# Optimization experiments

Hardware: AMD Instinct MI355X
Metric: run time of the kernel (lower is better)

## Reference

```python
import jax, jax.numpy as jnp
import numpy as np

B, S, D, H = 4, 2048, 512, 8
HD = D // H
POOL_HEADS = 8


def setup_inputs() -> dict:
    key = jax.random.key(0)
    ks = iter(jax.random.split(key, 32))
    p = {}
    p['x'] = jax.random.normal(next(ks), (B, S, D), dtype=jnp.float32)
    p['mask'] = jnp.zeros((B, S), dtype=jnp.float32)  # key_padding_mask (1.0 = padded)
    s = 1.0 / np.sqrt(D)
    for layer in ('1', '2'):
        for name in ('q', 'k', 'v', 'o'):
            p[f'{name}{layer}_w'] = jax.random.normal(next(ks), (D, D), dtype=jnp.float32) * s
            p[f'{name}{layer}_b'] = jnp.zeros((D,), dtype=jnp.float32)
    p['ln1_g'] = jnp.ones((D,), jnp.float32); p['ln1_b'] = jnp.zeros((D,), jnp.float32)
    p['ffn_w1'] = jax.random.normal(next(ks), (D, D), dtype=jnp.float32) * s
    p['ffn_b1'] = jnp.zeros((D,), jnp.float32)
    p['ffn_w2'] = jax.random.normal(next(ks), (D, D), dtype=jnp.float32) * s
    p['ffn_b2'] = jnp.zeros((D,), jnp.float32)
    p['ln2_g'] = jnp.ones((D,), jnp.float32); p['ln2_b'] = jnp.zeros((D,), jnp.float32)
    p['pool_w'] = jax.random.normal(next(ks), (D, POOL_HEADS), dtype=jnp.float32) * s
    p['pool_b'] = jnp.zeros((POOL_HEADS,), jnp.float32)
    return p


def _layernorm(x, g, b, eps=1e-5):
    mu = jnp.mean(x, axis=-1, keepdims=True)
    var = jnp.var(x, axis=-1, keepdims=True)
    return (x - mu) * jax.lax.rsqrt(var + eps) * g + b


def _mha(x, mask, qw, qb, kw, kb, vw, vb, ow, ob):
    b, s, d = x.shape
    q = (x @ qw + qb).reshape(b, s, H, HD)
    k = (x @ kw + kb).reshape(b, s, H, HD)
    v = (x @ vw + vb).reshape(b, s, H, HD)
    scores = jnp.einsum('bihd,bjhd->bhij', q, k) / jnp.sqrt(jnp.float32(HD))
    scores = scores - mask[:, None, None, :] * 1e30  # key_padding_mask
    w = jax.nn.softmax(scores, axis=-1)  # dropout is identity at eval
    out = jnp.einsum('bhij,bjhd->bihd', w, v).reshape(b, s, d)
    return out @ ow + ob


def _pool(x, mask, pw, pb):
    alpha = jax.nn.leaky_relu(x @ pw + pb)            # [B,S,POOL_HEADS]
    alpha = alpha + mask[:, :, None] * -1e16
    alpha = jax.nn.softmax(alpha, axis=1)             # softmax over sequence
    # sum over heads of alpha_h * x, then sum over sequence
    return jnp.einsum('bs,bsd->bd', alpha.sum(axis=-1), x)


def reference(x, mask,
              q1_w, q1_b, k1_w, k1_b, v1_w, v1_b, o1_w, o1_b,
              q2_w, q2_b, k2_w, k2_b, v2_w, v2_b, o2_w, o2_b,
              ln1_g, ln1_b, ffn_w1, ffn_b1, ffn_w2, ffn_b2,
              ln2_g, ln2_b, pool_w, pool_b):
    # F.normalize(x, p=2, dim=-1)
    x = x / jnp.maximum(jnp.linalg.norm(x, axis=-1, keepdims=True), 1e-12)
    h = _mha(x, mask, q1_w, q1_b, k1_w, k1_b, v1_w, v1_b, o1_w, o1_b)
    h = _layernorm(h, ln1_g, ln1_b)
    h = jax.nn.relu(h @ ffn_w1 + ffn_b1) @ ffn_w2 + ffn_b2
    h = _mha(h, mask, q2_w, q2_b, k2_w, k2_b, v2_w, v2_b, o2_w, o2_b)
    h = _layernorm(h, ln2_g, ln2_b)
    return _pool(h, mask, pool_w, pool_b)  # [B, D] patch_feature (cls=False -> logit is None)
```

## Files before the change

### kernel.cpp

```cpp
#include <hip/hip_runtime.h>
#include <hip/hip_bf16.h>
#include <stdint.h>

#define DEVI __device__ __forceinline__

typedef float f32x4 __attribute__((ext_vector_type(4)));
typedef float f32x16 __attribute__((ext_vector_type(16)));
typedef short bf16x8 __attribute__((ext_vector_type(8)));

typedef __attribute__((address_space(3))) unsigned int as3_u32;
typedef __attribute__((address_space(1))) unsigned int as1_u32;

DEVI void gload16(const void* g, void* l) {
  __builtin_amdgcn_global_load_lds((const as1_u32*)g, (as3_u32*)l, 16, 0, 0);
}

DEVI unsigned short bf16r(float f) {
  union { float f; unsigned int u; } v; v.f = f;
  unsigned int u = v.u;
  return (unsigned short)((u + 0x7FFFu + ((u >> 16) & 1u)) >> 16);
}

DEVI float bf2f(unsigned short u) {
  unsigned int x = ((unsigned int)u) << 16;
  union { unsigned int u; float f; } v; v.u = x;
  return v.f;
}

DEVI unsigned int pkbf16(float a, float b) {
  __hip_bfloat162 h = __float22bfloat162_rn(make_float2(a, b));
  return *(unsigned int*)&h;
}

struct PrepArgs {
  const float* w[10];
  const float* b1[3];
  const float* b2[3];
};

__global__ __launch_bounds__(256) void prep_kernel(PrepArgs pa, unsigned short* wt,
                                                   float* qb1, float* qb2) {
  __shared__ float lt[64][65];
  const int slot = blockIdx.z;
  const int n0 = blockIdx.x * 64, k0 = blockIdx.y * 64;
  const float* W = pa.w[slot];
  for (int it = 0; it < 16; it++) {
    int idx = it * 256 + threadIdx.x;
    int kr = idx >> 6, nc = idx & 63;
    lt[kr][nc] = W[(long)(k0 + kr) * 512 + n0 + nc];
  }
  __syncthreads();
  unsigned short* dst = wt + (long)slot * 512 * 512;
  for (int it = 0; it < 16; it++) {
    int idx = it * 256 + threadIdx.x;
    int nr = idx >> 6, kc = idx & 63;
    dst[(long)(n0 + nr) * 512 + k0 + kc] = bf16r(lt[kc][nr]);
  }
  if (blockIdx.x == 0 && blockIdx.y == 0) {
    if (slot < 3) {
      for (int i = threadIdx.x; i < 512; i += 256) qb1[slot * 512 + i] = pa.b1[slot][i];
    } else if (slot >= 6 && slot < 9) {
      for (int i = threadIdx.x; i < 512; i += 256) qb2[(slot - 6) * 512 + i] = pa.b2[slot - 6][i];
    }
  }
}

__global__ __launch_bounds__(256) void l2norm_kernel(const float* __restrict__ x,
                                                     unsigned short* __restrict__ xn) {
  const long row = blockIdx.x;
  const float* xr = x + row * 512;
  float v0 = xr[threadIdx.x], v1 = xr[threadIdx.x + 256];
  float ss = v0 * v0 + v1 * v1;
  #pragma unroll
  for (int off = 32; off > 0; off >>= 1) ss += __shfl_down(ss, off, 64);
  __shared__ float red[4];
  __shared__ float sc[1];
  int w = threadIdx.x >> 6, ln = threadIdx.x & 63;
  if (ln == 0) red[w] = ss;
  __syncthreads();
  if (threadIdx.x == 0) {
    float S = red[0] + red[1] + red[2] + red[3];
    sc[0] = 1.0f / fmaxf(sqrtf(S), 1e-12f);
  }
  __syncthreads();
  float s = sc[0];
  xn[row * 512 + threadIdx.x] = bf16r(v0 * s);
  xn[row * 512 + threadIdx.x + 256] = bf16r(v1 * s);
}

template <int EPI>
__global__ __launch_bounds__(256) void gemm_bt(const unsigned short* __restrict__ A,
                                               const unsigned short* __restrict__ Bt,
                                               const float* __restrict__ bias,
                                               void* __restrict__ Cv, int K, int N,
                                               unsigned short* __restrict__ vtout) {
  __shared__ unsigned short ldsA[128 * 64];
  __shared__ unsigned short ldsB[128 * 64];
  const int tid = threadIdx.x, w = tid >> 6, ln = tid & 63;
  const int bm = blockIdx.x, bn = blockIdx.y;
  const int wm = (w >> 1) * 64, wn = (w & 1) * 64;
  const f32x4 zf = {0.f, 0.f, 0.f, 0.f};
  f32x4 acc[4][4];
  #pragma unroll
  for (int i = 0; i < 4; i++)
    #pragma unroll
    for (int j = 0; j < 4; j++) acc[i][j] = zf;
  const int r8 = ln >> 3, s8 = ln & 7;
  for (int kt = 0; kt < K; kt += 64) {
    #pragma unroll
    for (int i = 0; i < 4; i++) {
      int row = w * 32 + i * 8 + r8;
      gload16(A + (long)(bm * 128 + row) * K + kt + s8 * 8, &ldsA[(w * 32 + i * 8) * 64]);
      gload16(Bt + (long)(bn * 128 + row) * K + kt + s8 * 8, &ldsB[(w * 32 + i * 8) * 64]);
    }
    __syncthreads();
    #pragma unroll
    for (int kk = 0; kk < 2; kk++) {
      bf16x8 af[4], bfr[4];
      #pragma unroll
      for (int mf = 0; mf < 4; mf++) {
        int row = wm + mf * 16 + (ln & 15);
        af[mf] = *(const bf16x8*)&ldsA[row * 64 + kk * 32 + (ln >> 4) * 8];
      }
      #pragma unroll
      for (int nf = 0; nf < 4; nf++) {
        int row = wn + nf * 16 + (ln & 15);
        bfr[nf] = *(const bf16x8*)&ldsB[row * 64 + kk * 32 + (ln >> 4) * 8];
      }
      #pragma unroll
      for (int mf = 0; mf < 4; mf++)
        #pragma unroll
        for (int nf = 0; nf < 4; nf++)
          acc[mf][nf] = __builtin_amdgcn_mfma_f32_16x16x32_bf16(af[mf], bfr[nf], acc[mf][nf], 0, 0, 0);
    }
    __syncthreads();
  }
  const int g = ln >> 4, c = ln & 15;
  #pragma unroll
  for (int mf = 0; mf < 4; mf++) {
    #pragma unroll
    for (int nf = 0; nf < 4; nf++) {
      int col = bn * 128 + wn + nf * 16 + c;
      float bv = bias[col];
      if (EPI == 3 && col >= 1024) {
        long row0 = bm * 128 + wm + mf * 16 + g * 4;
        int b = (int)(row0 >> 11), s = (int)(row0 & 2047);
        int vc = col - 1024, h = vc >> 6, hd = vc & 63;
        ushort4 o;
        o.x = bf16r(acc[mf][nf][0] + bv);
        o.y = bf16r(acc[mf][nf][1] + bv);
        o.z = bf16r(acc[mf][nf][2] + bv);
        o.w = bf16r(acc[mf][nf][3] + bv);
        *(ushort4*)(vtout + ((long)((b * 8 + h) * 64 + hd)) * 2048 + s) = o;
      } else {
        #pragma unroll
        for (int j = 0; j < 4; j++) {
          long row = bm * 128 + wm + mf * 16 + g * 4 + j;
          float v = acc[mf][nf][j] + bv;
          if (EPI == 2) v = v > 0.f ? v : 0.f;
          if (EPI == 0)
            ((float*)Cv)[row * N + col] = v;
          else
            ((unsigned short*)Cv)[row * N + col] = bf16r(v);
        }
      }
    }
  }
}

template <int EPI>
__global__ __launch_bounds__(256) void gemm_bt64(const unsigned short* __restrict__ A,
                                                 const unsigned short* __restrict__ Bt,
                                                 const float* __restrict__ bias,
                                                 void* __restrict__ Cv, int K, int N) {
  __shared__ unsigned short ldsA[128 * 64];
  __shared__ unsigned short ldsB[64 * 64];
  const int tid = threadIdx.x, w = tid >> 6, ln = tid & 63;
  const int bm = blockIdx.x, bn = blockIdx.y;
  const int wm = (w >> 1) * 64, wn = (w & 1) * 32;
  const f32x4 zf = {0.f, 0.f, 0.f, 0.f};
  f32x4 acc[4][2];
  #pragma unroll
  for (int i = 0; i < 4; i++)
    #pragma unroll
    for (int j = 0; j < 2; j++) acc[i][j] = zf;
  const int r8 = ln >> 3, s8 = ln & 7;
  for (int kt = 0; kt < K; kt += 64) {
    #pragma unroll
    for (int i = 0; i < 6; i++) {
      int jj = w * 6 + i;
      if (jj < 16) {
        gload16(A + (long)(bm * 128 + jj * 8 + r8) * K + kt + s8 * 8, &ldsA[jj * 512]);
      } else {
        int jb = jj - 16;
        gload16(Bt + (long)(bn * 64 + jb * 8 + r8) * K + kt + s8 * 8, &ldsB[jb * 512]);
      }
    }
    __syncthreads();
    #pragma unroll
    for (int kk = 0; kk < 2; kk++) {
      bf16x8 af[4], bfr[2];
      #pragma unroll
      for (int mf = 0; mf < 4; mf++)
        af[mf] = *(const bf16x8*)&ldsA[(wm + mf * 16 + (ln & 15)) * 64 + kk * 32 + (ln >> 4) * 8];
      #pragma unroll
      for (int nf = 0; nf < 2; nf++)
        bfr[nf] = *(const bf16x8*)&ldsB[(wn + nf * 16 + (ln & 15)) * 64 + kk * 32 + (ln >> 4) * 8];
      #pragma unroll
      for (int mf = 0; mf < 4; mf++)
        #pragma unroll
        for (int nf = 0; nf < 2; nf++)
          acc[mf][nf] = __builtin_amdgcn_mfma_f32_16x16x32_bf16(af[mf], bfr[nf], acc[mf][nf], 0, 0, 0);
    }
    __syncthreads();
  }
  const int g = ln >> 4, c = ln & 15;
  #pragma unroll
  for (int mf = 0; mf < 4; mf++) {
    #pragma unroll
    for (int nf = 0; nf < 2; nf++) {
      int col = bn * 64 + wn + nf * 16 + c;
      float bv = bias[col];
      #pragma unroll
      for (int j = 0; j < 4; j++) {
        long row = bm * 128 + wm + mf * 16 + g * 4 + j;
        float v = acc[mf][nf][j] + bv;
        if (EPI == 2) v = v > 0.f ? v : 0.f;
        if (EPI == 0)
          ((float*)Cv)[row * N + col] = v;
        else
          ((unsigned short*)Cv)[row * N + col] = bf16r(v);
      }
    }
  }
}

__global__ __launch_bounds__(256, 4) void attn_split_kernel(
    const unsigned short* __restrict__ qkv,
    const unsigned short* __restrict__ vt,
    const float* __restrict__ mask,
    unsigned short* __restrict__ opart,
    float* __restrict__ lpart) {
  const int tid = threadIdx.x, w = tid >> 6, ln = tid & 63;
  const int lo = ln & 31, hi = ln >> 5;
  const int bid = blockIdx.x + 16 * blockIdx.y + 512 * blockIdx.z;
  const int swz = (bid & 7) * 128 + (bid >> 3);
  const int qb = swz & 15, bh = (swz >> 4) & 31, sp = swz >> 9;
  const int b = bh >> 3, h = bh & 7;
  const int q0 = qb * 128 + w * 32;
  const unsigned short* qp = qkv + (long)(b * 2048) * 1536 + h * 64;
  const unsigned short* kp = qp + 512;
  const unsigned short* vtp = vt + (long)bh * 64 * 2048;
  const float* mp = mask + b * 2048;

  __shared__ unsigned short kbuf[2][32 * 64];
  __shared__ unsigned short vbuf[2][64 * 32];

  const int jj0 = w * 2;
  auto stage = [&](int buf, int kt) {
    #pragma unroll
    for (int u = 0; u < 2; u++) {
      int jj = jj0 + u;
      if (jj < 4) {
        int r = jj * 8 + (ln >> 3);
        int s = ln & 7;
        gload16(kp + (long)(kt + r) * 1536 + ((s ^ (r & 7)) * 8),
                &kbuf[buf][jj * 512]);
      } else {
        int j = jj - 4;
        int r = j * 16 + (ln >> 2);
        int s = ln & 3;
        gload16(vtp + (long)r * 2048 + kt + ((s ^ ((r >> 1) & 3)) * 8),
                &vbuf[buf][j * 512]);
      }
    }
  };

  bf16x8 qf[4];
  #pragma unroll
  for (int t = 0; t < 4; t++)
    qf[t] = *(const bf16x8*)(qp + (long)(q0 + lo) * 1536 + t * 16 + hi * 8);

  f32x16 oacc[2];
  #pragma unroll
  for (int t = 0; t < 2; t++)
    #pragma unroll
    for (int r = 0; r < 16; r++) oacc[t][r] = 0.f;
  float lsum = 0.f;
  const f32x16 zf16 = oacc[0];

  const int kt0 = sp * 1024;
  stage(0, kt0);
  __syncthreads();

  for (int it = 0; it < 32; it++) {
    const int kt = kt0 + it * 32;
    const int cur = it & 1;
    if (it + 1 < 32) stage(cur ^ 1, kt + 32);
    float mval = mp[kt + lo];
    f32x16 sacc = zf16;
    #pragma unroll
    for (int t = 0; t < 4; t++) {
      bf16x8 kf = *(const bf16x8*)&kbuf[cur][lo * 64 + (((t * 2 + hi) ^ (lo & 7)) * 8)];
      sacc = __builtin_amdgcn_mfma_f32_32x32x16_bf16(kf, qf[t], sacc, 0, 0, 0);
    }
    const float SC = 0.18033688011112042f;
    float e[16];
    if (__any(mval != 0.f)) {
      #pragma unroll
      for (int r = 0; r < 16; r++) {
        float mk = __shfl(mval, (r & 3) + 8 * (r >> 2) + 4 * hi, 64);
        e[r] = __builtin_amdgcn_exp2f(sacc[r] * SC - 1.4426950408889634e30f * mk);
      }
    } else {
      #pragma unroll
      for (int r = 0; r < 16; r++)
        e[r] = __builtin_amdgcn_exp2f(sacc[r] * SC);
    }
    #pragma unroll
    for (int r = 0; r < 16; r++) lsum += e[r];
    unsigned int cv[8];
    #pragma unroll
    for (int i = 0; i < 8; i++) cv[i] = pkbf16(e[2 * i], e[2 * i + 1]);
    #pragma unroll
    for (int stt = 0; stt < 2; stt++) {
      unsigned int c0 = cv[stt * 4 + 0], c1 = cv[stt * 4 + 1];
      unsigned int c2 = cv[stt * 4 + 2], c3 = cv[stt * 4 + 3];
      unsigned int s0 = __shfl_xor(c0, 32, 64), s1 = __shfl_xor(c1, 32, 64);
      unsigned int s2 = __shfl_xor(c2, 32, 64), s3 = __shfl_xor(c3, 32, 64);
      unsigned int pf[4];
      pf[0] = hi ? s2 : c0;
      pf[1] = hi ? s3 : c1;
      pf[2] = hi ? c2 : s0;
      pf[3] = hi ? c3 : s1;
      bf16x8 pfr = *(const bf16x8*)pf;
      #pragma unroll
      for (int tau = 0; tau < 2; tau++) {
        int vr = tau * 32 + lo;
        bf16x8 vf = *(const bf16x8*)&vbuf[cur][vr * 32 + ((((stt * 2 + hi) ^ ((vr >> 1) & 3))) * 8)];
        oacc[tau] = __builtin_amdgcn_mfma_f32_32x32x16_bf16(vf, pfr, oacc[tau], 0, 0, 0);
      }
    }
    __syncthreads();
  }
  lsum += __shfl_xor(lsum, 32, 64);
  unsigned short* ob = opart + (long)(sp * 32 + bh) * 2048 * 64;
  const long row = q0 + lo;
  #pragma unroll
  for (int tau = 0; tau < 2; tau++) {
    #pragma unroll
    for (int j = 0; j < 4; j++) {
      ushort4 o;
      o.x = bf16r(oacc[tau][4 * j + 0]);
      o.y = bf16r(oacc[tau][4 * j + 1]);
      o.z = bf16r(oacc[tau][4 * j + 2]);
      o.w = bf16r(oacc[tau][4 * j + 3]);
      *(ushort4*)(ob + row * 64 + tau * 32 + j * 8 + hi * 4) = o;
    }
  }
  if (hi == 0)
    lpart[(long)(sp * 32 + bh) * 2048 + row] = lsum;
}

__global__ __launch_bounds__(256) void attn_combine(const unsigned short* __restrict__ opart,
                                                    const float* __restrict__ lpart,
                                                    unsigned short* __restrict__ ao) {
  const long row = blockIdx.x;
  const int b = (int)(row >> 11), q = (int)(row & 2047);
  #pragma unroll
  for (int half = 0; half < 2; half++) {
    int col = threadIdx.x + half * 256;
    int h = col >> 6, hd = col & 63;
    int bh = b * 8 + h;
    float l = lpart[(long)bh * 2048 + q] + lpart[(long)(32 + bh) * 2048 + q];
    long i0 = ((long)bh * 2048 + q) * 64 + hd;
    long i1 = ((long)(32 + bh) * 2048 + q) * 64 + hd;
    float v = (bf2f(opart[i0]) + bf2f(opart[i1])) / l;
    ao[row * 512 + col] = bf16r(v);
  }
}

template <int OUTF>
__global__ __launch_bounds__(256) void ln_kernel(const float* __restrict__ in,
                                                 const float* __restrict__ gam,
                                                 const float* __restrict__ bet,
                                                 void* __restrict__ out) {
  const long row = blockIdx.x;
  const float* x = in + row * 512;
  float v0 = x[threadIdx.x], v1 = x[threadIdx.x + 256];
  float s = v0 + v1, ss = v0 * v0 + v1 * v1;
  #pragma unroll
  for (int off = 32; off > 0; off >>= 1) {
    s += __shfl_down(s, off, 64);
    ss += __shfl_down(ss, off, 64);
  }
  __shared__ float red[8];
  __shared__ float mv[2];
  int w = threadIdx.x >> 6, ln = threadIdx.x & 63;
  if (ln == 0) { red[w] = s; red[w + 4] = ss; }
  __syncthreads();
  if (threadIdx.x == 0) {
    float S = red[0] + red[1] + red[2] + red[3];
    float SS = red[4] + red[5] + red[6] + red[7];
    float mu = S * (1.f / 512.f);
    float var = SS * (1.f / 512.f) - mu * mu;
    mv[0] = mu;
    mv[1] = rsqrtf(var + 1e-5f);
  }
  __syncthreads();
  float mu = mv[0], rs = mv[1];
  float o0 = (v0 - mu) * rs * gam[threadIdx.x] + bet[threadIdx.x];
  float o1 = (v1 - mu) * rs * gam[threadIdx.x + 256] + bet[threadIdx.x + 256];
  if (OUTF == 0) {
    ((unsigned short*)out)[row * 512 + threadIdx.x] = bf16r(o0);
    ((unsigned short*)out)[row * 512 + threadIdx.x + 256] = bf16r(o1);
  } else {
    ((float*)out)[row * 512 + threadIdx.x] = o0;
    ((float*)out)[row * 512 + threadIdx.x + 256] = o1;
  }
}

__global__ __launch_bounds__(256) void alpha_kernel(const float* __restrict__ h,
                                                    const float* __restrict__ pw,
                                                    const float* __restrict__ pbias,
                                                    const float* __restrict__ mask,
                                                    float* __restrict__ alpha) {
  int w = threadIdx.x >> 6, ln = threadIdx.x & 63;
  long row = (long)blockIdx.x * 4 + w;
  float p[8];
  #pragma unroll
  for (int k = 0; k < 8; k++) p[k] = 0.f;
  #pragma unroll
  for (int it = 0; it < 8; it++) {
    int d = it * 64 + ln;
    float xv = h[row * 512 + d];
    const float* wr = pw + d * 8;
    #pragma unroll
    for (int k = 0; k < 8; k++) p[k] += xv * wr[k];
  }
  #pragma unroll
  for (int off = 32; off > 0; off >>= 1)
    #pragma unroll
    for (int k = 0; k < 8; k++) p[k] += __shfl_down(p[k], off, 64);
  if (ln == 0) {
    float mterm = mask[row] * (-1e16f);
    #pragma unroll
    for (int k = 0; k < 8; k++) {
      float a = p[k] + pbias[k];
      a = a < 0.f ? 0.01f * a : a;
      alpha[row * 8 + k] = a + mterm;
    }
  }
}

__global__ __launch_bounds__(256) void stats_kernel(const float* __restrict__ alpha,
                                                    float* __restrict__ stats) {
  int b = blockIdx.x >> 3, ph = blockIdx.x & 7;
  const float* a = alpha + (long)b * 2048 * 8 + ph;
  __shared__ float rr[4];
  __shared__ float mm[1];
  int w = threadIdx.x >> 6, ln = threadIdx.x & 63;
  float m = -1e38f;
  for (int s = threadIdx.x; s < 2048; s += 256) m = fmaxf(m, a[(long)s * 8]);
  #pragma unroll
  for (int off = 32; off > 0; off >>= 1) m = fmaxf(m, __shfl_down(m, off, 64));
  if (ln == 0) rr[w] = m;
  __syncthreads();
  if (threadIdx.x == 0) mm[0] = fmaxf(fmaxf(rr[0], rr[1]), fmaxf(rr[2], rr[3]));
  __syncthreads();
  float M = mm[0];
  float sum = 0.f;
  for (int s = threadIdx.x; s < 2048; s += 256) sum += __expf(a[(long)s * 8] - M);
  #pragma unroll
  for (int off = 32; off > 0; off >>= 1) sum += __shfl_down(sum, off, 64);
  __syncthreads();
  if (ln == 0) rr[w] = sum;
  __syncthreads();
  if (threadIdx.x == 0) {
    stats[blockIdx.x * 2] = M;
    stats[blockIdx.x * 2 + 1] = rr[0] + rr[1] + rr[2] + rr[3];
  }
}

__global__ __launch_bounds__(256) void pool_kernel(const float* __restrict__ h,
                                                   const float* __restrict__ alpha,
                                                   const float* __restrict__ stats,
                                                   float* __restrict__ partial) {
  int b = blockIdx.x >> 3, sc = blockIdx.x & 7;
  int s0 = sc * 256;
  __shared__ float wb[256];
  {
    long s = s0 + threadIdx.x;
    const float* a = alpha + ((long)b * 2048 + s) * 8;
    float wsum = 0.f;
    #pragma unroll
    for (int ph = 0; ph < 8; ph++) {
      float M = stats[(b * 8 + ph) * 2], Sm = stats[(b * 8 + ph) * 2 + 1];
      wsum += __expf(a[ph] - M) / Sm;
    }
    wb[threadIdx.x] = wsum;
  }
  __syncthreads();
  float a0 = 0.f, a1 = 0.f;
  const float* hb = h + ((long)b * 2048 + s0) * 512;
  for (int i = 0; i < 256; i++) {
    float wv = wb[i];
    a0 += wv * hb[(long)i * 512 + threadIdx.x];
    a1 += wv * hb[(long)i * 512 + threadIdx.x + 256];
  }
  partial[(long)blockIdx.x * 512 + threadIdx.x] = a0;
  partial[(long)blockIdx.x * 512 + threadIdx.x + 256] = a1;
}

__global__ __launch_bounds__(256) void pool_final(const float* __restrict__ partial,
                                                  float* __restrict__ out) {
  int b = blockIdx.x;
  float a0 = 0.f, a1 = 0.f;
  #pragma unroll
  for (int sc = 0; sc < 8; sc++) {
    a0 += partial[(long)(b * 8 + sc) * 512 + threadIdx.x];
    a1 += partial[(long)(b * 8 + sc) * 512 + threadIdx.x + 256];
  }
  out[b * 512 + threadIdx.x] = a0;
  out[b * 512 + threadIdx.x + 256] = a1;
}

extern "C" void kernel_launch(void* const* d_in, const int* in_sizes, int n_in,
                              void* d_out, int out_size, void* d_ws, size_t ws_size,
                              hipStream_t stream) {
  (void)in_sizes; (void)n_in; (void)out_size;
  if (ws_size < 92274688UL) return;

  const float* x    = (const float*)d_in[0];
  const float* mask = (const float*)d_in[1];
  const float* q1w = (const float*)d_in[2];  const float* q1b = (const float*)d_in[3];
  const float* k1w = (const float*)d_in[4];  const float* k1b = (const float*)d_in[5];
  const float* v1w = (const float*)d_in[6];  const float* v1b = (const float*)d_in[7];
  const float* o1w = (const float*)d_in[8];  const float* o1b = (const float*)d_in[9];
  const float* q2w = (const float*)d_in[10]; const float* q2b = (const float*)d_in[11];
  const float* k2w = (const float*)d_in[12]; const float* k2b = (const float*)d_in[13];
  const float* v2w = (const float*)d_in[14]; const float* v2b = (const float*)d_in[15];
  const float* o2w = (const float*)d_in[16]; const float* o2b = (const float*)d_in[17];
  const float* ln1g = (const float*)d_in[18]; const float* ln1b = (const float*)d_in[19];
  const float* fw1 = (const float*)d_in[20]; const float* fb1 = (const float*)d_in[21];
  const float* fw2 = (const float*)d_in[22]; const float* fb2 = (const float*)d_in[23];
  const float* ln2g = (const float*)d_in[24]; const float* ln2b = (const float*)d_in[25];
  const float* poolw = (const float*)d_in[26]; const float* poolb = (const float*)d_in[27];

  char* ws = (char*)d_ws;
  unsigned short* Wt  = (unsigned short*)(ws + 0);
  float* qb1          = (float*)(ws + 5242880);
  float* qb2          = (float*)(ws + 5249024);
  float* stats        = (float*)(ws + 5255168);
  float* alpha        = (float*)(ws + 5255424);
  float* partial      = (float*)(ws + 5517568);
  unsigned short* qkv = (unsigned short*)(ws + 8388608);
  unsigned short* vt  = (unsigned short*)(ws + 33554432);
  unsigned short* ao  = (unsigned short*)(ws + 41943040);
  float* t            = (float*)(ws + 50331648);
  unsigned short* xn  = (unsigned short*)(ws + 67108864);
  unsigned short* h1  = (unsigned short*)(ws + 75497472);
  unsigned short* f   = (unsigned short*)(ws + 83886080);
  unsigned short* h2  = xn;
  unsigned short* opart = (unsigned short*)(ws + 50331648);
  float* lpart          = (float*)(ws + 83886080);

  PrepArgs pa;
  pa.w[0] = q1w; pa.w[1] = k1w; pa.w[2] = v1w; pa.w[3] = o1w; pa.w[4] = fw1;
  pa.w[5] = fw2; pa.w[6] = q2w; pa.w[7] = k2w; pa.w[8] = v2w; pa.w[9] = o2w;
  pa.b1[0] = q1b; pa.b1[1] = k1b; pa.b1[2] = v1b;
  pa.b2[0] = q2b; pa.b2[1] = k2b; pa.b2[2] = v2b;

  prep_kernel<<<dim3(8, 8, 10), 256, 0, stream>>>(pa, Wt, qb1, qb2);
  l2norm_kernel<<<8192, 256, 0, stream>>>(x, xn);

  gemm_bt<3><<<dim3(64, 12), 256, 0, stream>>>(xn, Wt, qb1, qkv, 512, 1536, vt);
  attn_split_kernel<<<dim3(16, 32, 2), 256, 0, stream>>>(qkv, vt, mask, opart, lpart);
  attn_combine<<<8192, 256, 0, stream>>>(opart, lpart, ao);
  gemm_bt64<0><<<dim3(64, 8), 256, 0, stream>>>(ao, Wt + 3L * 512 * 512, o1b, t, 512, 512);
  ln_kernel<0><<<8192, 256, 0, stream>>>(t, ln1g, ln1b, h1);
  gemm_bt64<2><<<dim3(64, 8), 256, 0, stream>>>(h1, Wt + 4L * 512 * 512, fb1, f, 512, 512);
  gemm_bt64<1><<<dim3(64, 8), 256, 0, stream>>>(f, Wt + 5L * 512 * 512, fb2, h2, 512, 512);

  gemm_bt<3><<<dim3(64, 12), 256, 0, stream>>>(h2, Wt + 6L * 512 * 512, qb2, qkv, 512, 1536, vt);
  attn_split_kernel<<<dim3(16, 32, 2), 256, 0, stream>>>(qkv, vt, mask, opart, lpart);
  attn_combine<<<8192, 256, 0, stream>>>(opart, lpart, ao);
  gemm_bt64<0><<<dim3(64, 8), 256, 0, stream>>>(ao, Wt + 9L * 512 * 512, o2b, t, 512, 512);
  ln_kernel<1><<<8192, 256, 0, stream>>>(t, ln2g, ln2b, t);

  alpha_kernel<<<2048, 256, 0, stream>>>(t, poolw, poolb, mask, alpha);
  stats_kernel<<<32, 256, 0, stream>>>(alpha, stats);
  pool_kernel<<<32, 256, 0, stream>>>(t, alpha, stats, partial);
  pool_final<<<4, 256, 0, stream>>>(partial, (float*)d_out);
}
```

Before: 306.9 us.

## Hoist mask check, use explicit vmcnt waits, permlane32 swap in attention loop

Scans the key mask once before the attention loop instead of loading it and doing a wave vote every iteration. The per-iteration __syncthreads is replaced by an explicit s_waitcnt vmcnt on the async global-to-LDS loads plus raw s_barrier and sched_barrier fences, so the wait for the prefetched buffer happens only at the top of the next iteration. The cross-half shuffle of P fragments uses permlane32_swap when the compiler provides it. The hand-written vmcnt counts and scheduling fences are fragile: they must match the number of loads issued in flight, and they may prevent the compiler from reordering work.

```diff
diff --git a/kernel.cpp b/kernel.cpp
--- a/kernel.cpp
+++ b/kernel.cpp
@@ -276,6 +276,12 @@
     }
   };
 
+  const int kt0 = sp * 1024;
+  float mz = 0.f;
+  #pragma unroll
+  for (int i = 0; i < 16; i++) mz += fabsf(mp[kt0 + i * 64 + ln]);
+  const bool anymask = __any(mz != 0.f);
+
   bf16x8 qf[4];
   #pragma unroll
   for (int t = 0; t < 4; t++)
@@ -289,15 +295,19 @@
   float lsum = 0.f;
   const f32x16 zf16 = oacc[0];
 
-  const int kt0 = sp * 1024;
   stage(0, kt0);
-  __syncthreads();
 
   for (int it = 0; it < 32; it++) {
     const int kt = kt0 + it * 32;
     const int cur = it & 1;
-    if (it + 1 < 32) stage(cur ^ 1, kt + 32);
-    float mval = mp[kt + lo];
+    if (it + 1 < 32) {
+      stage(cur ^ 1, kt + 32);
+      asm volatile("s_waitcnt vmcnt(2)" ::: "memory");
+    } else {
+      asm volatile("s_waitcnt vmcnt(0)" ::: "memory");
+    }
+    __builtin_amdgcn_s_barrier();
+    __builtin_amdgcn_sched_barrier(0);
     f32x16 sacc = zf16;
     #pragma unroll
     for (int t = 0; t < 4; t++) {
@@ -306,17 +316,16 @@
     }
     const float SC = 0.18033688011112042f;
     float e[16];
-    if (__any(mval != 0.f)) {
-      #pragma unroll
-      for (int r = 0; r < 16; r++) {
-        float mk = __shfl(mval, (r & 3) + 8 * (r >> 2) + 4 * hi, 64);
-        e[r] = __builtin_amdgcn_exp2f(sacc[r] * SC - 1.4426950408889634e30f * mk);
-      }
-    } else {
+    #pragma unroll
+    for (int r = 0; r < 16; r++) e[r] = sacc[r] * SC;
+    if (anymask) {
+      float mval = mp[kt + lo];
       #pragma unroll
       for (int r = 0; r < 16; r++)
-        e[r] = __builtin_amdgcn_exp2f(sacc[r] * SC);
-    }
+        e[r] -= 1.4426950408889634e30f * __shfl(mval, (r & 3) + 8 * (r >> 2) + 4 * hi, 64);
+    }
+    #pragma unroll
+    for (int r = 0; r < 16; r++) e[r] = __builtin_amdgcn_exp2f(e[r]);
     #pragma unroll
     for (int r = 0; r < 16; r++) lsum += e[r];
     unsigned int cv[8];
@@ -324,15 +333,25 @@
     for (int i = 0; i < 8; i++) cv[i] = pkbf16(e[2 * i], e[2 * i + 1]);
     #pragma unroll
     for (int stt = 0; stt < 2; stt++) {
-      unsigned int c0 = cv[stt * 4 + 0], c1 = cv[stt * 4 + 1];
-      unsigned int c2 = cv[stt * 4 + 2], c3 = cv[stt * 4 + 3];
-      unsigned int s0 = __shfl_xor(c0, 32, 64), s1 = __shfl_xor(c1, 32, 64);
-      unsigned int s2 = __shfl_xor(c2, 32, 64), s3 = __shfl_xor(c3, 32, 64);
       unsigned int pf[4];
-      pf[0] = hi ? s2 : c0;
-      pf[1] = hi ? s3 : c1;
-      pf[2] = hi ? c2 : s0;
-      pf[3] = hi ? c3 : s1;
+#if __has_builtin(__builtin_amdgcn_permlane32_swap)
+      {
+        auto r0 = __builtin_amdgcn_permlane32_swap(cv[stt * 4 + 0], cv[stt * 4 + 2], false, false);
+        auto r1 = __builtin_amdgcn_permlane32_swap(cv[stt * 4 + 1], cv[stt * 4 + 3], false, false);
+        pf[0] = r0[0]; pf[1] = r1[0]; pf[2] = r0[1]; pf[3] = r1[1];
+      }
+#else
+      {
+        unsigned int c0 = cv[stt * 4 + 0], c1 = cv[stt * 4 + 1];
+        unsigned int c2 = cv[stt * 4 + 2], c3 = cv[stt * 4 + 3];
+        unsigned int s0 = __shfl_xor(c0, 32, 64), s1 = __shfl_xor(c1, 32, 64);
+        unsigned int s2 = __shfl_xor(c2, 32, 64), s3 = __shfl_xor(c3, 32, 64);
+        pf[0] = hi ? s2 : c0;
+        pf[1] = hi ? s3 : c1;
+        pf[2] = hi ? c2 : s0;
+        pf[3] = hi ? c3 : s1;
+      }
+#endif
       bf16x8 pfr = *(const bf16x8*)pf;
       #pragma unroll
       for (int tau = 0; tau < 2; tau++) {
@@ -341,7 +360,8 @@
         oacc[tau] = __builtin_amdgcn_mfma_f32_32x32x16_bf16(vf, pfr, oacc[tau], 0, 0, 0);
       }
     }
-    __syncthreads();
+    __builtin_amdgcn_sched_barrier(0);
+    __builtin_amdgcn_s_barrier();
   }
   lsum += __shfl_xor(lsum, 32, 64);
   unsigned short* ob = opart + (long)(sp * 32 + bh) * 2048 * 64;
```

New measurement: 303.5 us. Within noise of the previous version (-1.1%).

## Split attention keys four ways and hand-pipeline the K/V staging loop

Applied to the files above, without the earlier changes.

The attention kernel now splits the key range into four chunks of 512 instead of two of 1024, doubling the grid. The combine kernel sums four partial outputs and row sums. The inner loop is unrolled by two with fixed K/V buffers, explicit vmcnt waits and raw barriers, so the prefetch of the next tile overlaps the MFMAs. The mask chunk is preloaded into LDS once per block with a block-wide any-mask flag, and the cross-half shuffle is replaced by permlane32_swap. The risks are extra partial-output traffic and combine work, and correctness that depends on hand-placed waitcnt and barrier ordering.

```diff
diff --git a/kernel.cpp b/kernel.cpp
--- a/kernel.cpp
+++ b/kernel.cpp
@@ -244,7 +244,7 @@
   const int tid = threadIdx.x, w = tid >> 6, ln = tid & 63;
   const int lo = ln & 31, hi = ln >> 5;
   const int bid = blockIdx.x + 16 * blockIdx.y + 512 * blockIdx.z;
-  const int swz = (bid & 7) * 128 + (bid >> 3);
+  const int swz = (bid & 7) * 256 + (bid >> 3);
   const int qb = swz & 15, bh = (swz >> 4) & 31, sp = swz >> 9;
   const int b = bh >> 3, h = bh & 7;
   const int q0 = qb * 128 + w * 32;
@@ -252,29 +252,55 @@
   const unsigned short* kp = qp + 512;
   const unsigned short* vtp = vt + (long)bh * 64 * 2048;
   const float* mp = mask + b * 2048;
-
-  __shared__ unsigned short kbuf[2][32 * 64];
-  __shared__ unsigned short vbuf[2][64 * 32];
+  const int kt0 = sp * 512;
+
+  __shared__ unsigned short sbuf[2][4096];
+  __shared__ float mbuf[512];
+  __shared__ int mflag;
+
+  {
+    float mv0 = mp[kt0 + tid], mv1 = mp[kt0 + 256 + tid];
+    mbuf[tid] = mv0;
+    mbuf[tid + 256] = mv1;
+    if (tid == 0) mflag = 0;
+    __syncthreads();
+    if (mv0 != 0.f || mv1 != 0.f) mflag = 1;
+    __syncthreads();
+  }
+  const bool anymask = (mflag != 0);
 
   const int jj0 = w * 2;
-  auto stage = [&](int buf, int kt) {
-    #pragma unroll
-    for (int u = 0; u < 2; u++) {
-      int jj = jj0 + u;
-      if (jj < 4) {
-        int r = jj * 8 + (ln >> 3);
-        int s = ln & 7;
-        gload16(kp + (long)(kt + r) * 1536 + ((s ^ (r & 7)) * 8),
-                &kbuf[buf][jj * 512]);
-      } else {
-        int j = jj - 4;
-        int r = j * 16 + (ln >> 2);
-        int s = ln & 3;
-        gload16(vtp + (long)r * 2048 + kt + ((s ^ ((r >> 1) & 3)) * 8),
-                &vbuf[buf][j * 512]);
-      }
-    }
-  };
+  const char *src0, *src1;
+  long step;
+  if (w < 2) {
+    int r0 = jj0 * 8 + (ln >> 3), r1 = r0 + 8, s = ln & 7;
+    src0 = (const char*)kp + 2L * ((long)(kt0 + r0) * 1536 + ((s ^ (r0 & 7)) * 8));
+    src1 = (const char*)kp + 2L * ((long)(kt0 + r1) * 1536 + ((s ^ (r1 & 7)) * 8));
+    step = 32L * 1536 * 2;
+  } else {
+    int j0 = (w - 2) * 2;
+    int r0 = j0 * 16 + (ln >> 2), r1 = r0 + 16, s = ln & 3;
+    src0 = (const char*)vtp + 2L * ((long)r0 * 2048 + kt0 + ((s ^ ((r0 >> 1) & 3)) * 8));
+    src1 = (const char*)vtp + 2L * ((long)r1 * 2048 + kt0 + ((s ^ ((r1 >> 1) & 3)) * 8));
+    step = 64;
+  }
+  unsigned short* const d0a = &sbuf[0][jj0 * 512];
+  unsigned short* const d0b = d0a + 512;
+  unsigned short* const d1a = &sbuf[1][jj0 * 512];
+  unsigned short* const d1b = d1a + 512;
+
+  int koffe[4];
+  #pragma unroll
+  for (int t = 0; t < 4; t++)
+    koffe[t] = lo * 64 + (((t * 2 + hi) ^ (lo & 7)) * 8);
+  int voffe[4];
+  #pragma unroll
+  for (int stt = 0; stt < 2; stt++)
+    #pragma unroll
+    for (int tau = 0; tau < 2; tau++) {
+      int vr = tau * 32 + lo;
+      voffe[stt * 2 + tau] = 2048 + vr * 32 + ((((stt * 2 + hi) ^ ((vr >> 1) & 3))) * 8);
+    }
 
   bf16x8 qf[4];
   #pragma unroll
@@ -288,61 +314,74 @@
     for (int r = 0; r < 16; r++) oacc[t][r] = 0.f;
   float lsum = 0.f;
   const f32x16 zf16 = oacc[0];
-
-  const int kt0 = sp * 1024;
-  stage(0, kt0);
-  __syncthreads();
-
-  for (int it = 0; it < 32; it++) {
-    const int kt = kt0 + it * 32;
-    const int cur = it & 1;
-    if (it + 1 < 32) stage(cur ^ 1, kt + 32);
-    float mval = mp[kt + lo];
-    f32x16 sacc = zf16;
-    #pragma unroll
-    for (int t = 0; t < 4; t++) {
-      bf16x8 kf = *(const bf16x8*)&kbuf[cur][lo * 64 + (((t * 2 + hi) ^ (lo & 7)) * 8)];
-      sacc = __builtin_amdgcn_mfma_f32_32x32x16_bf16(kf, qf[t], sacc, 0, 0, 0);
-    }
-    const float SC = 0.18033688011112042f;
-    float e[16];
-    if (__any(mval != 0.f)) {
-      #pragma unroll
-      for (int r = 0; r < 16; r++) {
-        float mk = __shfl(mval, (r & 3) + 8 * (r >> 2) + 4 * hi, 64);
-        e[r] = __builtin_amdgcn_exp2f(sacc[r] * SC - 1.4426950408889634e30f * mk);
-      }
-    } else {
-      #pragma unroll
-      for (int r = 0; r < 16; r++)
-        e[r] = __builtin_amdgcn_exp2f(sacc[r] * SC);
-    }
-    #pragma unroll
-    for (int r = 0; r < 16; r++) lsum += e[r];
-    unsigned int cv[8];
-    #pragma unroll
-    for (int i = 0; i < 8; i++) cv[i] = pkbf16(e[2 * i], e[2 * i + 1]);
-    #pragma unroll
-    for (int stt = 0; stt < 2; stt++) {
-      unsigned int c0 = cv[stt * 4 + 0], c1 = cv[stt * 4 + 1];
-      unsigned int c2 = cv[stt * 4 + 2], c3 = cv[stt * 4 + 3];
-      unsigned int s0 = __shfl_xor(c0, 32, 64), s1 = __shfl_xor(c1, 32, 64);
-      unsigned int s2 = __shfl_xor(c2, 32, 64), s3 = __shfl_xor(c3, 32, 64);
-      unsigned int pf[4];
-      pf[0] = hi ? s2 : c0;
-      pf[1] = hi ? s3 : c1;
-      pf[2] = hi ? c2 : s0;
-      pf[3] = hi ? c3 : s1;
-      bf16x8 pfr = *(const bf16x8*)pf;
-      #pragma unroll
-      for (int tau = 0; tau < 2; tau++) {
-        int vr = tau * 32 + lo;
-        bf16x8 vf = *(const bf16x8*)&vbuf[cur][vr * 32 + ((((stt * 2 + hi) ^ ((vr >> 1) & 3))) * 8)];
-        oacc[tau] = __builtin_amdgcn_mfma_f32_32x32x16_bf16(vf, pfr, oacc[tau], 0, 0, 0);
-      }
-    }
-    __syncthreads();
-  }
+  const float SC = 0.18033688011112042f;
+
+  gload16(src0, d0a);
+  gload16(src1, d0b);
+  src0 += step; src1 += step;
+
+#define ATTN_BODY(CURB, DA, DB, ITOFF, STAGE_NEXT)                              \
+  {                                                                             \
+    if (STAGE_NEXT) {                                                           \
+      gload16(src0, DA);                                                        \
+      gload16(src1, DB);                                                        \
+      src0 += step; src1 += step;                                               \
+      asm volatile("s_waitcnt vmcnt(2)" ::: "memory");                          \
+    } else {                                                                    \
+      asm volatile("s_waitcnt vmcnt(0)" ::: "memory");                          \
+    }                                                                           \
+    __builtin_amdgcn_s_barrier();                                               \
+    __builtin_amdgcn_sched_barrier(0);                                          \
+    f32x16 sacc = zf16;                                                         \
+    _Pragma("unroll")                                                           \
+    for (int t = 0; t < 4; t++) {                                               \
+      bf16x8 kf = *(const bf16x8*)&sbuf[CURB][koffe[t]];                        \
+      sacc = __builtin_amdgcn_mfma_f32_32x32x16_bf16(kf, qf[t], sacc, 0, 0, 0); \
+    }                                                                           \
+    float e[16];                                                                \
+    _Pragma("unroll")                                                           \
+    for (int r = 0; r < 16; r++) e[r] = sacc[r] * SC;                           \
+    if (anymask) {                                                              \
+      float mval = mbuf[(ITOFF) + lo];                                          \
+      _Pragma("unroll")                                                         \
+      for (int r = 0; r < 16; r++)                                              \
+        e[r] -= 1.4426950408889634e30f *                                        \
+                __shfl(mval, (r & 3) + 8 * (r >> 2) + 4 * hi, 64);              \
+    }                                                                           \
+    _Pragma("unroll")                                                           \
+    for (int r = 0; r < 16; r++) e[r] = __builtin_amdgcn_exp2f(e[r]);           \
+    _Pragma("unroll")                                                           \
+    for (int r = 0; r < 16; r++) lsum += e[r];                                  \
+    unsigned int cv[8];                                                         \
+    _Pragma("unroll")                                                           \
+    for (int i = 0; i < 8; i++) cv[i] = pkbf16(e[2 * i], e[2 * i + 1]);         \
+    _Pragma("unroll")                                                           \
+    for (int stt = 0; stt < 2; stt++) {                                         \
+      unsigned int pf[4];                                                       \
+      {                                                                         \
+        auto r0_ = __builtin_amdgcn_permlane32_swap(cv[stt * 4 + 0],            \
+                                                    cv[stt * 4 + 2], false, false); \
+        auto r1_ = __builtin_amdgcn_permlane32_swap(cv[stt * 4 + 1],            \
+                                                    cv[stt * 4 + 3], false, false); \
+        pf[0] = r0_[0]; pf[1] = r1_[0]; pf[2] = r0_[1]; pf[3] = r1_[1];         \
+      }                                                                         \
+      bf16x8 pfr = *(const bf16x8*)pf;                                          \
+      _Pragma("unroll")                                                         \
+      for (int tau = 0; tau < 2; tau++) {                                       \
+        bf16x8 vf = *(const bf16x8*)&sbuf[CURB][voffe[stt * 2 + tau]];          \
+        oacc[tau] = __builtin_amdgcn_mfma_f32_32x32x16_bf16(vf, pfr, oacc[tau], 0, 0, 0); \
+      }                                                                         \
+    }                                                                           \
+    __builtin_amdgcn_sched_barrier(0);                                          \
+    __builtin_amdgcn_s_barrier();                                               \
+  }
+
+  for (int it2 = 0; it2 < 8; it2++) {
+    ATTN_BODY(0, d1a, d1b, it2 * 64, 1)
+    ATTN_BODY(1, d0a, d0b, it2 * 64 + 32, (it2 < 7))
+  }
+#undef ATTN_BODY
+
   lsum += __shfl_xor(lsum, 32, 64);
   unsigned short* ob = opart + (long)(sp * 32 + bh) * 2048 * 64;
   const long row = q0 + lo;
@@ -372,11 +411,13 @@
     int col = threadIdx.x + half * 256;
     int h = col >> 6, hd = col & 63;
     int bh = b * 8 + h;
-    float l = lpart[(long)bh * 2048 + q] + lpart[(long)(32 + bh) * 2048 + q];
-    long i0 = ((long)bh * 2048 + q) * 64 + hd;
-    long i1 = ((long)(32 + bh) * 2048 + q) * 64 + hd;
-    float v = (bf2f(opart[i0]) + bf2f(opart[i1])) / l;
-    ao[row * 512 + col] = bf16r(v);
+    float l = 0.f, v = 0.f;
+    #pragma unroll
+    for (int sp = 0; sp < 4; sp++) {
+      l += lpart[(long)(sp * 32 + bh) * 2048 + q];
+      v += bf2f(opart[((long)(sp * 32 + bh) * 2048 + q) * 64 + hd]);
+    }
+    ao[row * 512 + col] = bf16r(v / l);
   }
 }
 
@@ -575,7 +616,7 @@
   l2norm_kernel<<<8192, 256, 0, stream>>>(x, xn);
 
   gemm_bt<3><<<dim3(64, 12), 256, 0, stream>>>(xn, Wt, qb1, qkv, 512, 1536, vt);
-  attn_split_kernel<<<dim3(16, 32, 2), 256, 0, stream>>>(qkv, vt, mask, opart, lpart);
+  attn_split_kernel<<<dim3(16, 32, 4), 256, 0, stream>>>(qkv, vt, mask, opart, lpart);
   attn_combine<<<8192, 256, 0, stream>>>(opart, lpart, ao);
   gemm_bt64<0><<<dim3(64, 8), 256, 0, stream>>>(ao, Wt + 3L * 512 * 512, o1b, t, 512, 512);
   ln_kernel<0><<<8192, 256, 0, stream>>>(t, ln1g, ln1b, h1);
@@ -583,7 +624,7 @@
   gemm_bt64<1><<<dim3(64, 8), 256, 0, stream>>>(f, Wt + 5L * 512 * 512, fb2, h2, 512, 512);
 
   gemm_bt<3><<<dim3(64, 12), 256, 0, stream>>>(h2, Wt + 6L * 512 * 512, qb2, qkv, 512, 1536, vt);
-  attn_split_kernel<<<dim3(16, 32, 2), 256, 0, stream>>>(qkv, vt, mask, opart, lpart);
+  attn_split_kernel<<<dim3(16, 32, 4), 256, 0, stream>>>(qkv, vt, mask, opart, lpart);
   attn_combine<<<8192, 256, 0, stream>>>(opart, lpart, ao);
   gemm_bt64<0><<<dim3(64, 8), 256, 0, stream>>>(ao, Wt + 9L * 512 * 512, o2b, t, 512, 512);
   ln_kernel<1><<<8192, 256, 0, stream>>>(t, ln2g, ln2b, t);
```

After: 297.9 us. -2.9%, faster.
